# Performance work log

Hardware: AMD Instinct MI355X
Metric: run time of the kernel (lower is better)

Reference implementation:

```python
import math
import jax, jax.numpy as jnp
import numpy as np

T_MIN = 0.1
T_MAX = 1.0


def _log_cond_prob(energy, text_mask, mel_mask, direction, neg):
    # energy: (B, I, J); returns (B, I, J, K) with K=J (alpha) or J-1 (beta)
    B, I, J = energy.shape
    if direction == 'alpha':
        K = J
        tri_jk = jnp.arange(J)[:, None] >= jnp.arange(K)[None, :]  # torch triu: valid if j >= k
    else:
        K = J - 1
        tri_jk = jnp.arange(J)[:, None] <= jnp.arange(K)[None, :]  # torch tril: valid if j <= k
    tm = text_mask[:, :, None, None]           # (B,I,1,1)
    mmj = mel_mask[:, None, :, None]           # (B,1,J,1)
    mmk = mel_mask[:, None, None, :K]          # (B,1,1,K)
    mask = tm & mmj & mmk                      # (B,I,J,K)
    tri = tri_jk[None, None] & mask
    mask_invalid = jnp.broadcast_to(tm & mmk, (B, I, J, K))
    text_invalid = jnp.broadcast_to(tm, (B, I, J, K))
    right_mask = mask | (~mask_invalid)
    e = jnp.broadcast_to(energy[..., None], (B, I, J, K))
    e = jnp.where((~tri) & mask_invalid, neg, e)
    e = jnp.where(~mask_invalid, -10.0, e)
    e = e - jax.nn.logsumexp(e, axis=2, keepdims=True)  # normalize over mel dim j
    e = jnp.where(~mask_invalid, neg, e)
    e = jnp.where(~right_mask, -10.0, e)
    e = jnp.where(~text_invalid, -10.0, e)
    return e


def _roll(x, shifts, axis):
    # per-batch roll of x along `axis` by shifts[b]
    return jax.vmap(lambda xb, s: jnp.roll(xb, s, axis=axis - 1))(x, shifts)


def _right_shift(x, sh_t, sh_m):
    x = _roll(x, sh_t, 1)
    x = _roll(x, sh_m, 2)
    return _roll(x, sh_m.at[1:].add(-1), 3)  # faithful to in-place shifts_mel_dim[1:] -= 1


def _left_shift(x, sh_t, sh_m):
    x = x[..., None]
    x = _roll(x, -sh_t, 1)
    x = _roll(x, -sh_m, 2)
    return x[..., 0]


def _compute_alpha(lcp_a, neg):
    # alpha[:, i, j] = lse_k(alpha[:, i-1, k] + lcp_a[:, i-1, j-1, k]) for j >= i
    B, I, J, _ = lcp_a.shape
    j_idx = jnp.arange(J + 1)
    row0 = jnp.full((B, J + 1), neg, dtype=lcp_a.dtype).at[:, 0].set(0.0)

    def step(prev, xs):  # prev = alpha[:, i-1, :J]
        lcp_i, i = xs
        new = jax.nn.logsumexp(prev[:, None, :] + lcp_i, axis=2)  # (B, J), index j-1
        row = jnp.concatenate([jnp.full((B, 1), neg, dtype=new.dtype), new], axis=1)
        row = jnp.where(j_idx[None, :] >= i, row, neg)
        return row[:, :J], row

    _, rows = jax.lax.scan(step, row0[:, :J], (jnp.swapaxes(lcp_a, 0, 1), jnp.arange(1, I + 1)))
    return jnp.concatenate([row0[:, None, :], jnp.swapaxes(rows, 0, 1)], axis=1)  # (B, I+1, J+1)


def _compute_beta(lcp_b, neg):
    # beta[:, i, j] = lse_k(beta[:, i+1, k+1] + lcp_b[:, i, j, k]) for j < J+i-I+1
    B, I, J, _ = lcp_b.shape
    j_idx = jnp.arange(J)
    last = jnp.full((B, J), neg, dtype=lcp_b.dtype).at[:, J - 1].set(0.0)

    def step(nxt, xs):
        lcp_i, i = xs
        full = jax.nn.logsumexp(nxt[:, 1:][:, None, :] + lcp_i, axis=2)  # (B, J)
        row = jnp.where(j_idx[None, :] < (J + i - I + 1), full, neg)
        return row, row

    _, rows = jax.lax.scan(step, last, (jnp.swapaxes(lcp_b[:, :I - 1], 0, 1), jnp.arange(I - 1)), reverse=True)
    return jnp.concatenate([jnp.swapaxes(rows, 0, 1), last[:, None, :]], axis=1)  # (B, I, J)


def _forward(text_embeddings, mel_embeddings, text_mask, mel_mask, noise, temperature_ratio, neg):
    B, I, Dt = text_embeddings.shape
    _, J, Dm = mel_embeddings.shape
    energy = jnp.einsum('bid,bjd->bij', text_embeddings, mel_embeddings) / math.sqrt(Dt * Dm)
    temp = T_MIN + (T_MAX - T_MIN) * temperature_ratio[0]
    energy = (energy - jnp.log(-jnp.log(noise))) / temp  # Gumbel noise + temperature
    lcp_a = _log_cond_prob(energy, text_mask, mel_mask, 'alpha', neg)
    alpha = _compute_alpha(lcp_a, neg)
    t_len = text_mask.sum(1)
    m_len = mel_mask.sum(1)
    sh_t = t_len.max() - t_len
    sh_m = m_len.max() - m_len
    lcp_b = _log_cond_prob(energy, text_mask, mel_mask, 'beta', neg)
    lcp_b = _right_shift(lcp_b, sh_t, sh_m)
    beta = _compute_beta(lcp_b, neg)
    beta = _left_shift(beta, sh_t, sh_m)
    gamma = alpha[:, 1:, 1:] + beta
    gamma_mask = text_mask[:, :, None] & mel_mask[:, None, :]
    gls_mask = jnp.broadcast_to(text_mask[:, :, None], (B, I, J)) | gamma_mask
    gamma = jnp.where(gls_mask, gamma, neg)
    gamma = gamma - jax.nn.logsumexp(gamma, axis=1, keepdims=True)  # normalize over text dim
    gamma = jnp.where(gamma_mask, gamma, neg)
    expanded = jnp.einsum('bij,bid->bjd', jnp.exp(gamma), text_embeddings)
    expanded = expanded * mel_mask[:, :, None]
    return gamma, expanded


def setup_inputs() -> dict:
    key = jax.random.key(0)
    k1, k2, k3, k4 = jax.random.split(key, 4)
    B, I, J, Dt, Dm = 1, 128, 640, 256, 256
    text_embeddings = jax.random.normal(k1, (B, I, Dt), dtype=jnp.float32)
    mel_embeddings = jax.random.normal(k2, (B, J, Dm), dtype=jnp.float32)
    text_mask = jnp.ones((B, I), dtype=bool)
    mel_mask = jnp.ones((B, J), dtype=bool)
    noise = jnp.clip(jax.random.uniform(k3, (B, I, J), dtype=jnp.float32), 1e-8, 1.0 - 1e-8)
    temperature_ratio = jax.random.uniform(k4, (1,), dtype=jnp.float32)
    return {
        'text_embeddings': text_embeddings,
        'mel_embeddings': mel_embeddings,
        'text_mask': text_mask,
        'mel_mask': mel_mask,
        'noise': noise,
        'temperature_ratio': temperature_ratio,
    }


def reference(text_embeddings, mel_embeddings, text_mask, mel_mask, noise, temperature_ratio):
    return _forward(text_embeddings, mel_embeddings, text_mask, mel_mask, noise, temperature_ratio, -jnp.inf)
```

## Files before the change

kernel.cpp:

```cpp
#include <hip/hip_runtime.h>
#include <math.h>

constexpr int TI = 128;
constexpr int TJ = 640;
constexpr int TD = 256;
constexpr int EPL = 10;
constexpr int NS  = 3;
constexpr int CH  = 4;
constexpr int NP  = 6;

#define NEG (-1e30f)
#define LOG2E 1.44269504088896340736f
#define LN2   0.69314718055994530942f

__device__ __forceinline__ float rexp2(float x) { return __builtin_amdgcn_exp2f(x); }
__device__ __forceinline__ float rlog2(float x) { return __builtin_amdgcn_logf(x); }

struct MS { float m, s; };
__device__ __forceinline__ MS ms_combine(MS a, MS b) {
    float d = b.m - a.m;
    bool al = d <= 0.0f;
    float m = al ? a.m : b.m;
    float t = rexp2(al ? d : -d);
    float s = al ? fmaf(b.s, t, a.s) : fmaf(a.s, t, b.s);
    return {m, s};
}
__device__ __forceinline__ MS ms_push(MS run, float x) { return ms_combine(run, {x, 1.0f}); }
__device__ __forceinline__ float ms_final(MS a) {
    return (a.m < -1e29f) ? NEG : a.m + rlog2(a.s);
}

template<int CTRL, int RMASK>
__device__ __forceinline__ float dpp_f(float src, float oldv) {
    int r = __builtin_amdgcn_update_dpp(
        __float_as_int(oldv), __float_as_int(src), CTRL, RMASK, 0xF, false);
    return __int_as_float(r);
}
template<int CTRL, int RMASK>
__device__ __forceinline__ MS dpp_ms(MS v) {
    MS t;
    t.m = dpp_f<CTRL, RMASK>(v.m, NEG);
    t.s = dpp_f<CTRL, RMASK>(v.s, 0.0f);
    return t;
}
__device__ __forceinline__ MS wave_incl_scan_ms(MS v) {
    v = ms_combine(dpp_ms<0x111, 0xF>(v), v);
    v = ms_combine(dpp_ms<0x112, 0xF>(v), v);
    v = ms_combine(dpp_ms<0x114, 0xF>(v), v);
    v = ms_combine(dpp_ms<0x118, 0xF>(v), v);
    v = ms_combine(dpp_ms<0x142, 0xA>(v), v);
    v = ms_combine(dpp_ms<0x143, 0xC>(v), v);
    return v;
}
__device__ __forceinline__ MS wave_excl_from_incl_ms(MS incl) {
    return dpp_ms<0x138, 0xF>(incl);
}
__device__ __forceinline__ float wave_incl_scan_add(float v) {
    v += dpp_f<0x111, 0xF>(v, 0.0f);
    v += dpp_f<0x112, 0xF>(v, 0.0f);
    v += dpp_f<0x114, 0xF>(v, 0.0f);
    v += dpp_f<0x118, 0xF>(v, 0.0f);
    v += dpp_f<0x142, 0xA>(v, 0.0f);
    v += dpp_f<0x143, 0xC>(v, 0.0f);
    return v;
}
__device__ __forceinline__ float wave_incl_scan_max(float v) {
    v = fmaxf(v, dpp_f<0x111, 0xF>(v, NEG));
    v = fmaxf(v, dpp_f<0x112, 0xF>(v, NEG));
    v = fmaxf(v, dpp_f<0x114, 0xF>(v, NEG));
    v = fmaxf(v, dpp_f<0x118, 0xF>(v, NEG));
    v = fmaxf(v, dpp_f<0x142, 0xA>(v, NEG));
    v = fmaxf(v, dpp_f<0x143, 0xC>(v, NEG));
    return v;
}
__device__ __forceinline__ float readlane63(float v) {
    return __int_as_float(__builtin_amdgcn_readlane(__float_as_int(v), 63));
}
__device__ __forceinline__ float readlaneN(float v, int n) {
    return __int_as_float(__builtin_amdgcn_readlane(__float_as_int(v), n));
}

__device__ __forceinline__ void cbar() { asm volatile("" ::: "memory"); }
__device__ __forceinline__ int opaque_zero(int v) {
    int r;
    asm("v_xor_b32 %0, %1, %1" : "=v"(r) : "v"(v));
    return r;
}
__device__ __forceinline__ int pollwait(volatile int* flag, int need) {
    int rv;
    do { rv = *flag; } while (rv < need);
    return rv;
}

__device__ __forceinline__ void load10(float* d, const float* s) {
    const float2* p = (const float2*)s;
    #pragma unroll
    for (int k = 0; k < 5; k++) { float2 v = p[k]; d[2*k] = v.x; d[2*k+1] = v.y; }
}
__device__ __forceinline__ void store10(float* d, const float* v) {
    float2* p = (float2*)d;
    #pragma unroll
    for (int k = 0; k < 5; k++) { float2 t; t.x = v[2*k]; t.y = v[2*k+1]; p[k] = t; }
}

__global__ __launch_bounds__(256) void k_melT(
        const float* __restrict__ mel, float* __restrict__ melT) {
    __shared__ float ldsT[64][65];
    int j0 = blockIdx.x * 64, c0 = blockIdx.y * 64, tid = threadIdx.x;
    int rr = tid >> 4, c4 = tid & 15;
    #pragma unroll
    for (int p = 0; p < 4; p++) {
        int r = p * 16 + rr;
        float4 v = *(const float4*)(mel + (size_t)(j0 + r) * TD + c0 + c4 * 4);
        ldsT[c4 * 4 + 0][r] = v.x;
        ldsT[c4 * 4 + 1][r] = v.y;
        ldsT[c4 * 4 + 2][r] = v.z;
        ldsT[c4 * 4 + 3][r] = v.w;
    }
    __syncthreads();
    int jj = tid & 63, cw = tid >> 6;
    #pragma unroll
    for (int p = 0; p < 16; p++) {
        int cc = p * 4 + cw;
        melT[(size_t)(c0 + cc) * TJ + j0 + jj] = ldsT[cc][jj];
    }
}

__global__ __launch_bounds__(640) void k_energy(
        const float* __restrict__ text, const float* __restrict__ melT,
        const float* __restrict__ noise, const float* __restrict__ trat,
        float* __restrict__ energy, float* __restrict__ Ga,
        float* __restrict__ Gb, float* __restrict__ Cst) {
    __shared__ float trowm[TD], trowc[TD], trowp[TD];
    __shared__ float erowm[TJ], erowc[TJ], erowp[TJ];
    __shared__ float pcur[TJ], scur[TJ];
    __shared__ float wred[2][EPL];
    int i = blockIdx.x, tid = threadIdx.x;
    if (tid < TD) {
        trowc[tid] = text[i * TD + tid];
        trowm[tid] = (i > 0)      ? text[(i - 1) * TD + tid] : 0.0f;
        trowp[tid] = (i < TI - 1) ? text[(i + 1) * TD + tid] : 0.0f;
    }
    __syncthreads();
    float temp = 0.1f + 0.9f * trat[0];
    float sc = LOG2E / temp;
    int j = tid;
    float am = 0.0f, ac = 0.0f, ap = 0.0f;
    #pragma unroll 8
    for (int c = 0; c < TD; c++) {
        float m = melT[(size_t)c * TJ + j];
        am = fmaf(trowm[c], m, am);
        ac = fmaf(trowc[c], m, ac);
        ap = fmaf(trowp[c], m, ap);
    }
    float gm = (i > 0)      ? logf(-logf(noise[(i - 1) * TJ + j])) : 0.0f;
    float gc =                logf(-logf(noise[i * TJ + j]));
    float gp = (i < TI - 1) ? logf(-logf(noise[(i + 1) * TJ + j])) : 0.0f;
    erowm[j] = (am * (1.0f / 256.0f) - gm) * sc;
    float e2 = (ac * (1.0f / 256.0f) - gc) * sc;
    erowc[j] = e2;
    erowp[j] = (ap * (1.0f / 256.0f) - gp) * sc;
    energy[i * TJ + j] = e2;
    __syncthreads();
    if (tid < 64) {
        int l = tid;
        MS loc = {NEG, 0.0f};
        #pragma unroll
        for (int q = 0; q < EPL; q++) loc = ms_push(loc, erowc[l * EPL + q]);
        MS off = wave_excl_from_incl_ms(wave_incl_scan_ms(loc));
        MS run = off;
        #pragma unroll
        for (int q = 0; q < EPL; q++) {
            run = ms_push(run, erowc[l * EPL + q]);
            pcur[l * EPL + q] = ms_final(run);
        }
        loc = {NEG, 0.0f};
        #pragma unroll
        for (int q = 0; q < EPL; q++) loc = ms_push(loc, erowc[TJ - 1 - (l * EPL + q)]);
        off = wave_excl_from_incl_ms(wave_incl_scan_ms(loc));
        run = off;
        #pragma unroll
        for (int q = 0; q < EPL; q++) {
            int idx = TJ - 1 - (l * EPL + q);
            run = ms_push(run, erowc[idx]);
            scur[idx] = ms_final(run);
        }
    }
    __syncthreads();
    float ga, gb;
    if (i == 0) ga = (j == 0) ? -scur[0] : NEG;
    else        ga = (j == 0) ? NEG : erowm[j - 1] - scur[j];
    bool has_b = (i <= TI - 2);
    if (has_b) {
        if (i == TI - 2) gb = (j == 1) ? -pcur[TJ - 2] : NEG;
        else             gb = (j == 0) ? NEG : erowp[TJ - j] - pcur[TJ - 1 - j];
    } else gb = NEG;
    int wv = tid >> 6, l = tid & 63;
    float ma = readlane63(wave_incl_scan_max(ga));
    float mb = readlane63(wave_incl_scan_max(gb));
    if (l == 0) { wred[0][wv] = ma; wred[1][wv] = mb; }
    __syncthreads();
    float Ca = wred[0][0], Cb = wred[1][0];
    #pragma unroll
    for (int k = 1; k < EPL; k++) {
        Ca = fmaxf(Ca, wred[0][k]);
        Cb = fmaxf(Cb, wred[1][k]);
    }
    Ga[i * TJ + j] = rexp2(ga - Ca);
    if (has_b) Gb[i * TJ + j] = rexp2(gb - Cb);
    if (tid == 0) { Cst[i] = Ca; if (has_b) Cst[TI + i] = Cb; }
}

__global__ __launch_bounds__(320, 1) void k_scan(
        const float* __restrict__ energy, const float* __restrict__ Ga,
        const float* __restrict__ Gb, const float* __restrict__ Cst,
        float* __restrict__ a, float* __restrict__ b) {
    __shared__ float Gring[NS][CH][TJ];
    __shared__ float Ppring[NP][TJ + 8];
    __shared__ int ready[NS];
    __shared__ int prow, cdone, ocnt[2];
    const int tid = threadIdx.x, wave = tid >> 6, l = tid & 63;
    const bool is_alpha = (blockIdx.x == 0);
    const int nrows = is_alpha ? TI : TI - 1;
    const int nch = (nrows + CH - 1) / CH;
    if (tid < NS) ready[tid] = 0;
    if (tid == 0) { prow = 0; cdone = 0; ocnt[0] = 0; ocnt[1] = 0; }
    __syncthreads();

    if (wave == 0) {
        float C0, C1;
        if (is_alpha) { C0 = Cst[l]; C1 = Cst[64 + l]; }
        else          { C0 = Cst[128 + l]; C1 = Cst[192 + l]; }
        float Pp[EPL];
        #pragma unroll
        for (int q = 0; q < EPL; q++) Pp[q] = 0.0f;
        float rprev = 0.0f, Lam = 0.0f;
        int seen0 = 0, seen1 = 0;
        for (int c = 0; c < nch; c++) {
            int rv = pollwait(&ready[c % NS], c + 1);
            cbar();
            int tok = opaque_zero(rv);
            float Gr[CH][EPL];
            #pragma unroll
            for (int q = 0; q < CH; q++)
                if (c * CH + q < nrows)
                    load10(Gr[q], &Gring[c % NS][q][l * EPL + tok]);
            #pragma unroll
            for (int s = 0; s < CH; s++) {
                int t = c * CH + s;
                if (t < nrows) {
                    float lp[EPL];
                    if (t == 0) {
                        #pragma unroll
                        for (int q = 0; q < EPL; q++) lp[q] = Gr[0][q];
                    } else {
                        float carry = dpp_f<0x138, 0xF>(Pp[EPL - 1], 0.0f);
                        float rp = rprev;
                        lp[0] = carry * rp * Gr[s][0];
                        #pragma unroll
                        for (int q = 1; q < EPL; q++) lp[q] = Pp[q - 1] * rp * Gr[s][q];
                    }
                    #pragma unroll
                    for (int q = 9; q >= 1; q--) lp[q] += lp[q - 1];
                    #pragma unroll
                    for (int q = 9; q >= 2; q--) lp[q] += lp[q - 2];
                    #pragma unroll
                    for (int q = 9; q >= 4; q--) lp[q] += lp[q - 4];
                    #pragma unroll
                    for (int q = 9; q >= 8; q--) lp[q] += lp[q - 8];
                    float incl = wave_incl_scan_add(lp[EPL - 1]);
                    float excl = dpp_f<0x138, 0xF>(incl, 0.0f);
                    #pragma unroll
                    for (int q = 0; q < EPL; q++) Pp[q] = excl + lp[q];
                    float T = readlane63(incl);
                    int idx2 = is_alpha ? t : (126 - t);
                    float Cc = (idx2 < 64) ? readlaneN(C0, idx2) : readlaneN(C1, idx2 - 64);
                    float basev = Lam + Cc;
                    if (t >= NP) {
                        int need = ((t - NP) >> 1) + 1;
                        if (t & 1) {
                            if (seen1 < need) { seen1 = pollwait(&ocnt[1], need); cbar(); }
                        } else {
                            if (seen0 < need) { seen0 = pollwait(&ocnt[0], need); cbar(); }
                        }
                    }
                    int ps = t % NP;
                    store10(&Ppring[ps][l * EPL], Pp);
                    if (l == 0) Ppring[ps][TJ] = basev;
                    cbar();
                    if (l == 0) *(volatile int*)&prow = t + 1;
                    Lam = basev + rlog2(T);
                    rprev = (T > 0.0f) ? __builtin_amdgcn_rcpf(T) : 0.0f;
                }
            }
            cbar();
            if (l == 0) *(volatile int*)&cdone = c + 1;
        }
    } else if (wave <= 2) {
        const float* Gsrc = is_alpha ? Ga : Gb;
        for (int c = wave - 1; c < nch; c += 2) {
            if (c >= NS) { int dv = pollwait(&cdone, c - NS + 1); cbar(); (void)dv; }
            int slot = c % NS;
            int cnt = nrows - c * CH; if (cnt > CH) cnt = CH;
            int m0 = is_alpha ? c * CH : (TI - 2 - c * CH - (cnt - 1));
            const float4* src = (const float4*)(Gsrc + (size_t)m0 * TJ);
            int total4 = cnt * (TJ / 4);
            #pragma unroll
            for (int it = 0; it < CH * TJ / 4 / 64; it++) {
                int o4 = it * 64 + l;
                if (o4 < total4) {
                    float4 v = src[o4];
                    int ri = o4 / 160, c4 = o4 - ri * 160;
                    int s = is_alpha ? ri : (cnt - 1 - ri);
                    ((float4*)Gring[slot][s])[c4] = v;
                }
            }
            __threadfence_block();
            if (l == 0) *(volatile int*)&ready[slot] = c + 1;
        }
    } else {
        int w = wave - 3;
        if (!is_alpha && w == 0) {
            #pragma unroll
            for (int k = 0; k < EPL; k++) {
                int j = l + 64 * k;
                b[(TI - 1) * TJ + j] = (j == TJ - 1) ? 0.0f : NEG;
            }
        }
        for (int t = w; t < nrows; t += 2) {
            int row = is_alpha ? t : (TI - 2 - t);
            const float* Erow = energy + (size_t)row * TJ;
            float ev[EPL];
            #pragma unroll
            for (int k = 0; k < EPL; k++) ev[k] = Erow[l + 64 * k];
            int rv = pollwait(&prow, t + 1);
            cbar();
            int tok = opaque_zero(rv);
            int ps = t % NP;
            float base = Ppring[ps][TJ + tok];
            float ov[EPL];
            #pragma unroll
            for (int k = 0; k < EPL; k++) {
                int j = l + 64 * k;
                int pj = is_alpha ? j : (TJ - 1 - j);
                ov[k] = ev[k] + rlog2(Ppring[ps][pj + tok]) + base;
            }
            float* dst = (is_alpha ? a : b) + (size_t)row * TJ;
            #pragma unroll
            for (int k = 0; k < EPL; k++) dst[l + 64 * k] = ov[k];
            cbar();
            if (l == 0) *(volatile int*)&ocnt[w] = (t >> 1) + 1;
        }
    }
}

__global__ __launch_bounds__(256) void k_gamma(
        const float* __restrict__ a, const float* __restrict__ b,
        const float* __restrict__ text,
        float* __restrict__ outg, float* __restrict__ oute) {
    __shared__ float w128[TI];
    __shared__ float redm[2], reds[2];
    int j = blockIdx.x, tid = threadIdx.x;
    float gg = NEG;
    if (tid < TI) {
        float av = a[tid * TJ + j];
        float bv = b[tid * TJ + j];
        gg = (av < -1e29f || bv < -1e29f) ? NEG : av + bv;
        MS v = {gg, 1.0f};
        #pragma unroll
        for (int off = 32; off > 0; off >>= 1) {
            float om = __shfl_xor(v.m, off, 64);
            float os = __shfl_xor(v.s, off, 64);
            v = ms_combine(v, {om, os});
        }
        if ((tid & 63) == 0) { redm[tid >> 6] = v.m; reds[tid >> 6] = v.s; }
    }
    __syncthreads();
    float lse = ms_final(ms_combine({redm[0], reds[0]}, {redm[1], reds[1]}));
    if (tid < TI) {
        bool fin = gg > -1e29f;
        outg[tid * TJ + j] = fin ? (gg - lse) * LN2 : NEG;
        w128[tid] = fin ? rexp2(gg - lse) : 0.0f;
    }
    __syncthreads();
    float acc = 0.0f;
    #pragma unroll 8
    for (int ii = 0; ii < TI; ii++) acc += w128[ii] * text[ii * TD + tid];
    oute[(size_t)j * TD + tid] = acc;
}

extern "C" void kernel_launch(void* const* d_in, const int* in_sizes, int n_in,
                              void* d_out, int out_size, void* d_ws, size_t ws_size,
                              hipStream_t stream) {
    const float* text  = (const float*)d_in[0];
    const float* mel   = (const float*)d_in[1];
    const float* noise = (const float*)d_in[4];
    const float* trat  = (const float*)d_in[5];

    float* outg = (float*)d_out;
    float* oute = outg + TI * TJ;

    float* w      = (float*)d_ws;
    float* energy = w;
    float* Ga     = w + 1 * TI * TJ;
    float* Gb     = w + 2 * TI * TJ;
    float* Cst    = Gb + (size_t)(TI - 1) * TJ;
    float* melT   = w + 3 * TI * TJ;
    float* aArr   = w + 3 * TI * TJ;
    float* bArr   = w + 4 * TI * TJ;

    k_melT  <<<dim3(TJ / 64, TD / 64), 256, 0, stream>>>(mel, melT);
    k_energy<<<TI, TJ, 0, stream>>>(text, melT, noise, trat, energy, Ga, Gb, Cst);
    k_scan  <<<2, 320, 0, stream>>>(energy, Ga, Gb, Cst, aArr, bArr);
    k_gamma <<<TJ, 256, 0, stream>>>(aArr, bArr, text, outg, oute);
}
```

Before: 146.5 us.

## Move energy addition out of serial scan into gamma with transposed layouts

The scan kernel no longer loads energy rows and adds them. It writes only the log-sum part, transposed to j-major. The energy add and the boundary row of beta move into k_gamma, which now reads the transposed ET/LaT/LbT arrays contiguously per block instead of with stride TJ. This takes loads off the latency-critical two-block serial scan, but its stores become strided by TI (uncoalesced) and k_energy's energy store becomes strided too.

```diff
diff --git a/kernel.cpp b/kernel.cpp
--- a/kernel.cpp
+++ b/kernel.cpp
@@ -129,7 +129,7 @@
 __global__ __launch_bounds__(640) void k_energy(
         const float* __restrict__ text, const float* __restrict__ melT,
         const float* __restrict__ noise, const float* __restrict__ trat,
-        float* __restrict__ energy, float* __restrict__ Ga,
+        float* __restrict__ ET, float* __restrict__ Ga,
         float* __restrict__ Gb, float* __restrict__ Cst) {
     __shared__ float trowm[TD], trowc[TD], trowp[TD];
     __shared__ float erowm[TJ], erowc[TJ], erowp[TJ];
@@ -160,7 +160,7 @@
     float e2 = (ac * (1.0f / 256.0f) - gc) * sc;
     erowc[j] = e2;
     erowp[j] = (ap * (1.0f / 256.0f) - gp) * sc;
-    energy[i * TJ + j] = e2;
+    ET[(size_t)j * TI + i] = e2;
     __syncthreads();
     if (tid < 64) {
         int l = tid;
@@ -212,9 +212,9 @@
 }
 
 __global__ __launch_bounds__(320, 1) void k_scan(
-        const float* __restrict__ energy, const float* __restrict__ Ga,
-        const float* __restrict__ Gb, const float* __restrict__ Cst,
-        float* __restrict__ a, float* __restrict__ b) {
+        const float* __restrict__ Ga, const float* __restrict__ Gb,
+        const float* __restrict__ Cst,
+        float* __restrict__ LaT, float* __restrict__ LbT) {
     __shared__ float Gring[NS][CH][TJ];
     __shared__ float Ppring[NP][TJ + 8];
     __shared__ int ready[NS];
@@ -320,34 +320,20 @@
         }
     } else {
         int w = wave - 3;
-        if (!is_alpha && w == 0) {
-            #pragma unroll
-            for (int k = 0; k < EPL; k++) {
-                int j = l + 64 * k;
-                b[(TI - 1) * TJ + j] = (j == TJ - 1) ? 0.0f : NEG;
-            }
-        }
+        float* dst = is_alpha ? LaT : LbT;
         for (int t = w; t < nrows; t += 2) {
             int row = is_alpha ? t : (TI - 2 - t);
-            const float* Erow = energy + (size_t)row * TJ;
-            float ev[EPL];
-            #pragma unroll
-            for (int k = 0; k < EPL; k++) ev[k] = Erow[l + 64 * k];
             int rv = pollwait(&prow, t + 1);
             cbar();
             int tok = opaque_zero(rv);
             int ps = t % NP;
             float base = Ppring[ps][TJ + tok];
-            float ov[EPL];
             #pragma unroll
             for (int k = 0; k < EPL; k++) {
                 int j = l + 64 * k;
                 int pj = is_alpha ? j : (TJ - 1 - j);
-                ov[k] = ev[k] + rlog2(Ppring[ps][pj + tok]) + base;
+                dst[(size_t)j * TI + row] = rlog2(Ppring[ps][pj + tok]) + base;
             }
-            float* dst = (is_alpha ? a : b) + (size_t)row * TJ;
-            #pragma unroll
-            for (int k = 0; k < EPL; k++) dst[l + 64 * k] = ov[k];
             cbar();
             if (l == 0) *(volatile int*)&ocnt[w] = (t >> 1) + 1;
         }
@@ -355,16 +341,19 @@
 }
 
 __global__ __launch_bounds__(256) void k_gamma(
-        const float* __restrict__ a, const float* __restrict__ b,
-        const float* __restrict__ text,
+        const float* __restrict__ ET, const float* __restrict__ LaT,
+        const float* __restrict__ LbT, const float* __restrict__ text,
         float* __restrict__ outg, float* __restrict__ oute) {
     __shared__ float w128[TI];
     __shared__ float redm[2], reds[2];
     int j = blockIdx.x, tid = threadIdx.x;
     float gg = NEG;
     if (tid < TI) {
-        float av = a[tid * TJ + j];
-        float bv = b[tid * TJ + j];
+        float e2 = ET[(size_t)j * TI + tid];
+        float av = e2 + LaT[(size_t)j * TI + tid];
+        float bv;
+        if (tid == TI - 1) bv = (j == TJ - 1) ? 0.0f : NEG;
+        else               bv = e2 + LbT[(size_t)j * TI + tid];
         gg = (av < -1e29f || bv < -1e29f) ? NEG : av + bv;
         MS v = {gg, 1.0f};
         #pragma unroll
@@ -401,16 +390,16 @@
     float* oute = outg + TI * TJ;
 
     float* w      = (float*)d_ws;
-    float* energy = w;
+    float* ET     = w;
     float* Ga     = w + 1 * TI * TJ;
     float* Gb     = w + 2 * TI * TJ;
     float* Cst    = Gb + (size_t)(TI - 1) * TJ;
     float* melT   = w + 3 * TI * TJ;
-    float* aArr   = w + 3 * TI * TJ;
-    float* bArr   = w + 4 * TI * TJ;
+    float* LaT    = w + 3 * TI * TJ;
+    float* LbT    = w + 4 * TI * TJ;
 
     k_melT  <<<dim3(TJ / 64, TD / 64), 256, 0, stream>>>(mel, melT);
-    k_energy<<<TI, TJ, 0, stream>>>(text, melT, noise, trat, energy, Ga, Gb, Cst);
-    k_scan  <<<2, 320, 0, stream>>>(energy, Ga, Gb, Cst, aArr, bArr);
-    k_gamma <<<TJ, 256, 0, stream>>>(aArr, bArr, text, outg, oute);
-}
+    k_energy<<<TI, TJ, 0, stream>>>(text, melT, noise, trat, ET, Ga, Gb, Cst);
+    k_scan  <<<2, 320, 0, stream>>>(Ga, Gb, Cst, LaT, LbT);
+    k_gamma <<<TJ, 256, 0, stream>>>(ET, LaT, LbT, text, outg, oute);
+}
```

Measured after the change: 170.8 us. 16.6% more time.

## Merge four kernels into two using global-flag inter-block synchronization

Applied to the files above, without the earlier changes.

Folds the mel transpose into the energy kernel and the gamma pass into the scan kernel, with device-scope atomic flags and spin-waits replacing kernel boundaries. It also adds s_sleep back-off to the LDS poll loops. The aim is to remove two launch gaps and let noise log work overlap the transpose. The cost is a memset launch, and correctness depends on all blocks being co-resident so the spinning blocks cannot deadlock. Gamma blocks also sit idle while the serial scan runs.

```diff
diff --git a/kernel.cpp b/kernel.cpp
--- a/kernel.cpp
+++ b/kernel.cpp
@@ -8,6 +8,7 @@
 constexpr int NS  = 3;
 constexpr int CH  = 4;
 constexpr int NP  = 6;
+constexpr int GAMMA_BLKS = 254;
 
 #define NEG (-1e30f)
 #define LOG2E 1.44269504088896340736f
@@ -87,8 +88,8 @@
     return r;
 }
 __device__ __forceinline__ int pollwait(volatile int* flag, int need) {
-    int rv;
-    do { rv = *flag; } while (rv < need);
+    int rv = *flag;
+    while (rv < need) { __builtin_amdgcn_s_sleep(1); rv = *flag; }
     return rv;
 }
 
@@ -103,48 +104,63 @@
     for (int k = 0; k < 5; k++) { float2 t; t.x = v[2*k]; t.y = v[2*k+1]; p[k] = t; }
 }
 
-__global__ __launch_bounds__(256) void k_melT(
-        const float* __restrict__ mel, float* __restrict__ melT) {
-    __shared__ float ldsT[64][65];
-    int j0 = blockIdx.x * 64, c0 = blockIdx.y * 64, tid = threadIdx.x;
-    int rr = tid >> 4, c4 = tid & 15;
-    #pragma unroll
-    for (int p = 0; p < 4; p++) {
-        int r = p * 16 + rr;
-        float4 v = *(const float4*)(mel + (size_t)(j0 + r) * TD + c0 + c4 * 4);
-        ldsT[c4 * 4 + 0][r] = v.x;
-        ldsT[c4 * 4 + 1][r] = v.y;
-        ldsT[c4 * 4 + 2][r] = v.z;
-        ldsT[c4 * 4 + 3][r] = v.w;
-    }
-    __syncthreads();
-    int jj = tid & 63, cw = tid >> 6;
-    #pragma unroll
-    for (int p = 0; p < 16; p++) {
-        int cc = p * 4 + cw;
-        melT[(size_t)(c0 + cc) * TJ + j0 + jj] = ldsT[cc][jj];
-    }
-}
-
-__global__ __launch_bounds__(640) void k_energy(
-        const float* __restrict__ text, const float* __restrict__ melT,
+__global__ __launch_bounds__(640) void k_A(
+        const float* __restrict__ mel, const float* __restrict__ text,
         const float* __restrict__ noise, const float* __restrict__ trat,
-        float* __restrict__ energy, float* __restrict__ Ga,
-        float* __restrict__ Gb, float* __restrict__ Cst) {
+        float* __restrict__ melT, float* __restrict__ energy,
+        float* __restrict__ Ga, float* __restrict__ Gb,
+        float* __restrict__ Cst, int* __restrict__ flagA) {
+    int bid = blockIdx.x, tid = threadIdx.x;
+    if (bid < 40) {
+        __shared__ float ldsT[64][65];
+        int j0 = (bid % 10) * 64, c0 = (bid / 10) * 64;
+        #pragma unroll
+        for (int it = 0; it < 2; it++) {
+            int idx = it * 640 + tid;
+            if (idx < 1024) {
+                int r = idx >> 4, c4 = idx & 15;
+                float4 v = *(const float4*)(mel + (size_t)(j0 + r) * TD + c0 + c4 * 4);
+                ldsT[c4 * 4 + 0][r] = v.x;
+                ldsT[c4 * 4 + 1][r] = v.y;
+                ldsT[c4 * 4 + 2][r] = v.z;
+                ldsT[c4 * 4 + 3][r] = v.w;
+            }
+        }
+        __syncthreads();
+        #pragma unroll
+        for (int it = 0; it < 7; it++) {
+            int idx = it * 640 + tid;
+            if (idx < 4096) {
+                int cc = idx >> 6, jj = idx & 63;
+                melT[(size_t)(c0 + cc) * TJ + j0 + jj] = ldsT[cc][jj];
+            }
+        }
+        __threadfence();
+        __syncthreads();
+        if (tid == 0)
+            __hip_atomic_fetch_add(flagA, 1, __ATOMIC_RELEASE, __HIP_MEMORY_SCOPE_AGENT);
+        return;
+    }
     __shared__ float trowm[TD], trowc[TD], trowp[TD];
     __shared__ float erowm[TJ], erowc[TJ], erowp[TJ];
     __shared__ float pcur[TJ], scur[TJ];
     __shared__ float wred[2][EPL];
-    int i = blockIdx.x, tid = threadIdx.x;
+    int i = bid - 40, j = tid;
     if (tid < TD) {
         trowc[tid] = text[i * TD + tid];
         trowm[tid] = (i > 0)      ? text[(i - 1) * TD + tid] : 0.0f;
         trowp[tid] = (i < TI - 1) ? text[(i + 1) * TD + tid] : 0.0f;
     }
-    __syncthreads();
     float temp = 0.1f + 0.9f * trat[0];
     float sc = LOG2E / temp;
-    int j = tid;
+    float gm = (i > 0)      ? logf(-logf(noise[(i - 1) * TJ + j])) : 0.0f;
+    float gc =                logf(-logf(noise[i * TJ + j]));
+    float gp = (i < TI - 1) ? logf(-logf(noise[(i + 1) * TJ + j])) : 0.0f;
+    if (tid == 0) {
+        while (__hip_atomic_load(flagA, __ATOMIC_ACQUIRE, __HIP_MEMORY_SCOPE_AGENT) < 40)
+            __builtin_amdgcn_s_sleep(4);
+    }
+    __syncthreads();
     float am = 0.0f, ac = 0.0f, ap = 0.0f;
     #pragma unroll 8
     for (int c = 0; c < TD; c++) {
@@ -153,9 +169,6 @@
         ac = fmaf(trowc[c], m, ac);
         ap = fmaf(trowp[c], m, ap);
     }
-    float gm = (i > 0)      ? logf(-logf(noise[(i - 1) * TJ + j])) : 0.0f;
-    float gc =                logf(-logf(noise[i * TJ + j]));
-    float gp = (i < TI - 1) ? logf(-logf(noise[(i + 1) * TJ + j])) : 0.0f;
     erowm[j] = (am * (1.0f / 256.0f) - gm) * sc;
     float e2 = (ac * (1.0f / 256.0f) - gc) * sc;
     erowc[j] = e2;
@@ -211,182 +224,196 @@
     if (tid == 0) { Cst[i] = Ca; if (has_b) Cst[TI + i] = Cb; }
 }
 
-__global__ __launch_bounds__(320, 1) void k_scan(
+__global__ __launch_bounds__(320, 1) void k_B(
         const float* __restrict__ energy, const float* __restrict__ Ga,
         const float* __restrict__ Gb, const float* __restrict__ Cst,
-        float* __restrict__ a, float* __restrict__ b) {
-    __shared__ float Gring[NS][CH][TJ];
-    __shared__ float Ppring[NP][TJ + 8];
-    __shared__ int ready[NS];
-    __shared__ int prow, cdone, ocnt[2];
-    const int tid = threadIdx.x, wave = tid >> 6, l = tid & 63;
-    const bool is_alpha = (blockIdx.x == 0);
-    const int nrows = is_alpha ? TI : TI - 1;
-    const int nch = (nrows + CH - 1) / CH;
-    if (tid < NS) ready[tid] = 0;
-    if (tid == 0) { prow = 0; cdone = 0; ocnt[0] = 0; ocnt[1] = 0; }
-    __syncthreads();
-
-    if (wave == 0) {
-        float C0, C1;
-        if (is_alpha) { C0 = Cst[l]; C1 = Cst[64 + l]; }
-        else          { C0 = Cst[128 + l]; C1 = Cst[192 + l]; }
-        float Pp[EPL];
-        #pragma unroll
-        for (int q = 0; q < EPL; q++) Pp[q] = 0.0f;
-        float rprev = 0.0f, Lam = 0.0f;
-        int seen0 = 0, seen1 = 0;
-        for (int c = 0; c < nch; c++) {
-            int rv = pollwait(&ready[c % NS], c + 1);
-            cbar();
-            int tok = opaque_zero(rv);
-            float Gr[CH][EPL];
+        const float* __restrict__ text,
+        float* __restrict__ a, float* __restrict__ b,
+        float* __restrict__ outg, float* __restrict__ oute,
+        int* __restrict__ flagC) {
+    int bid = blockIdx.x, tid = threadIdx.x;
+    if (bid < 2) {
+        __shared__ float Gring[NS][CH][TJ];
+        __shared__ float Ppring[NP][TJ + 8];
+        __shared__ int ready[NS];
+        __shared__ int prow, cdone, ocnt[2];
+        const int wave = tid >> 6, l = tid & 63;
+        const bool is_alpha = (bid == 0);
+        const int nrows = is_alpha ? TI : TI - 1;
+        const int nch = (nrows + CH - 1) / CH;
+        if (tid < NS) ready[tid] = 0;
+        if (tid == 0) { prow = 0; cdone = 0; ocnt[0] = 0; ocnt[1] = 0; }
+        __syncthreads();
+
+        if (wave == 0) {
+            float C0, C1;
+            if (is_alpha) { C0 = Cst[l]; C1 = Cst[64 + l]; }
+            else          { C0 = Cst[128 + l]; C1 = Cst[192 + l]; }
+            float Pp[EPL];
             #pragma unroll
-            for (int q = 0; q < CH; q++)
-                if (c * CH + q < nrows)
-                    load10(Gr[q], &Gring[c % NS][q][l * EPL + tok]);
-            #pragma unroll
-            for (int s = 0; s < CH; s++) {
-                int t = c * CH + s;
-                if (t < nrows) {
-                    float lp[EPL];
-                    if (t == 0) {
+            for (int q = 0; q < EPL; q++) Pp[q] = 0.0f;
+            float rprev = 0.0f, Lam = 0.0f;
+            int seen0 = 0, seen1 = 0;
+            for (int c = 0; c < nch; c++) {
+                int rv = pollwait(&ready[c % NS], c + 1);
+                cbar();
+                int tok = opaque_zero(rv);
+                float Gr[CH][EPL];
+                #pragma unroll
+                for (int q = 0; q < CH; q++)
+                    if (c * CH + q < nrows)
+                        load10(Gr[q], &Gring[c % NS][q][l * EPL + tok]);
+                #pragma unroll
+                for (int s = 0; s < CH; s++) {
+                    int t = c * CH + s;
+                    if (t < nrows) {
+                        float lp[EPL];
+                        if (t == 0) {
+                            #pragma unroll
+                            for (int q = 0; q < EPL; q++) lp[q] = Gr[0][q];
+                        } else {
+                            float carry = dpp_f<0x138, 0xF>(Pp[EPL - 1], 0.0f);
+                            float rp = rprev;
+                            lp[0] = carry * rp * Gr[s][0];
+                            #pragma unroll
+                            for (int q = 1; q < EPL; q++) lp[q] = Pp[q - 1] * rp * Gr[s][q];
+                        }
                         #pragma unroll
-                        for (int q = 0; q < EPL; q++) lp[q] = Gr[0][q];
-                    } else {
-                        float carry = dpp_f<0x138, 0xF>(Pp[EPL - 1], 0.0f);
-                        float rp = rprev;
-                        lp[0] = carry * rp * Gr[s][0];
+                        for (int q = 9; q >= 1; q--) lp[q] += lp[q - 1];
                         #pragma unroll
-                        for (int q = 1; q < EPL; q++) lp[q] = Pp[q - 1] * rp * Gr[s][q];
+                        for (int q = 9; q >= 2; q--) lp[q] += lp[q - 2];
+                        #pragma unroll
+                        for (int q = 9; q >= 4; q--) lp[q] += lp[q - 4];
+                        #pragma unroll
+                        for (int q = 9; q >= 8; q--) lp[q] += lp[q - 8];
+                        float incl = wave_incl_scan_add(lp[EPL - 1]);
+                        float excl = dpp_f<0x138, 0xF>(incl, 0.0f);
+                        #pragma unroll
+                        for (int q = 0; q < EPL; q++) Pp[q] = excl + lp[q];
+                        float T = readlane63(incl);
+                        int idx2 = is_alpha ? t : (126 - t);
+                        float Cc = (idx2 < 64) ? readlaneN(C0, idx2) : readlaneN(C1, idx2 - 64);
+                        float basev = Lam + Cc;
+                        if (t >= NP) {
+                            int need = ((t - NP) >> 1) + 1;
+                            if (t & 1) {
+                                if (seen1 < need) { seen1 = pollwait(&ocnt[1], need); cbar(); }
+                            } else {
+                                if (seen0 < need) { seen0 = pollwait(&ocnt[0], need); cbar(); }
+                            }
+                        }
+                        int ps = t % NP;
+                        store10(&Ppring[ps][l * EPL], Pp);
+                        if (l == 0) Ppring[ps][TJ] = basev;
+                        cbar();
+                        if (l == 0) *(volatile int*)&prow = t + 1;
+                        Lam = basev + rlog2(T);
+                        rprev = (T > 0.0f) ? __builtin_amdgcn_rcpf(T) : 0.0f;
                     }
-                    #pragma unroll
-                    for (int q = 9; q >= 1; q--) lp[q] += lp[q - 1];
-                    #pragma unroll
-                    for (int q = 9; q >= 2; q--) lp[q] += lp[q - 2];
-                    #pragma unroll
-                    for (int q = 9; q >= 4; q--) lp[q] += lp[q - 4];
-                    #pragma unroll
-                    for (int q = 9; q >= 8; q--) lp[q] += lp[q - 8];
-                    float incl = wave_incl_scan_add(lp[EPL - 1]);
-                    float excl = dpp_f<0x138, 0xF>(incl, 0.0f);
-                    #pragma unroll
-                    for (int q = 0; q < EPL; q++) Pp[q] = excl + lp[q];
-                    float T = readlane63(incl);
-                    int idx2 = is_alpha ? t : (126 - t);
-                    float Cc = (idx2 < 64) ? readlaneN(C0, idx2) : readlaneN(C1, idx2 - 64);
-                    float basev = Lam + Cc;
-                    if (t >= NP) {
-                        int need = ((t - NP) >> 1) + 1;
-                        if (t & 1) {
-                            if (seen1 < need) { seen1 = pollwait(&ocnt[1], need); cbar(); }
-                        } else {
-                            if (seen0 < need) { seen0 = pollwait(&ocnt[0], need); cbar(); }
-                        }
+                }
+                cbar();
+                if (l == 0) *(volatile int*)&cdone = c + 1;
+            }
+        } else if (wave <= 2) {
+            const float* Gsrc = is_alpha ? Ga : Gb;
+            for (int c = wave - 1; c < nch; c += 2) {
+                if (c >= NS) { int dv = pollwait(&cdone, c - NS + 1); cbar(); (void)dv; }
+                int slot = c % NS;
+                int cnt = nrows - c * CH; if (cnt > CH) cnt = CH;
+                int m0 = is_alpha ? c * CH : (TI - 2 - c * CH - (cnt - 1));
+                const float4* src = (const float4*)(Gsrc + (size_t)m0 * TJ);
+                int total4 = cnt * (TJ / 4);
+                #pragma unroll
+                for (int it = 0; it < CH * TJ / 4 / 64; it++) {
+                    int o4 = it * 64 + l;
+                    if (o4 < total4) {
+                        float4 v = src[o4];
+                        int ri = o4 / 160, c4 = o4 - ri * 160;
+                        int s = is_alpha ? ri : (cnt - 1 - ri);
+                        ((float4*)Gring[slot][s])[c4] = v;
                     }
-                    int ps = t % NP;
-                    store10(&Ppring[ps][l * EPL], Pp);
-                    if (l == 0) Ppring[ps][TJ] = basev;
-                    cbar();
-                    if (l == 0) *(volatile int*)&prow = t + 1;
-                    Lam = basev + rlog2(T);
-                    rprev = (T > 0.0f) ? __builtin_amdgcn_rcpf(T) : 0.0f;
                 }
-            }
-            cbar();
-            if (l == 0) *(volatile int*)&cdone = c + 1;
-        }
-    } else if (wave <= 2) {
-        const float* Gsrc = is_alpha ? Ga : Gb;
-        for (int c = wave - 1; c < nch; c += 2) {
-            if (c >= NS) { int dv = pollwait(&cdone, c - NS + 1); cbar(); (void)dv; }
-            int slot = c % NS;
-            int cnt = nrows - c * CH; if (cnt > CH) cnt = CH;
-            int m0 = is_alpha ? c * CH : (TI - 2 - c * CH - (cnt - 1));
-            const float4* src = (const float4*)(Gsrc + (size_t)m0 * TJ);
-            int total4 = cnt * (TJ / 4);
-            #pragma unroll
-            for (int it = 0; it < CH * TJ / 4 / 64; it++) {
-                int o4 = it * 64 + l;
-                if (o4 < total4) {
-                    float4 v = src[o4];
-                    int ri = o4 / 160, c4 = o4 - ri * 160;
-                    int s = is_alpha ? ri : (cnt - 1 - ri);
-                    ((float4*)Gring[slot][s])[c4] = v;
+                __threadfence_block();
+                if (l == 0) *(volatile int*)&ready[slot] = c + 1;
+            }
+        } else {
+            int w = wave - 3;
+            if (!is_alpha && w == 0) {
+                #pragma unroll
+                for (int k = 0; k < EPL; k++) {
+                    int j = l + 64 * k;
+                    b[(TI - 1) * TJ + j] = (j == TJ - 1) ? 0.0f : NEG;
                 }
             }
-            __threadfence_block();
-            if (l == 0) *(volatile int*)&ready[slot] = c + 1;
-        }
-    } else {
-        int w = wave - 3;
-        if (!is_alpha && w == 0) {
-            #pragma unroll
-            for (int k = 0; k < EPL; k++) {
-                int j = l + 64 * k;
-                b[(TI - 1) * TJ + j] = (j == TJ - 1) ? 0.0f : NEG;
-            }
-        }
-        for (int t = w; t < nrows; t += 2) {
-            int row = is_alpha ? t : (TI - 2 - t);
-            const float* Erow = energy + (size_t)row * TJ;
-            float ev[EPL];
-            #pragma unroll
-            for (int k = 0; k < EPL; k++) ev[k] = Erow[l + 64 * k];
-            int rv = pollwait(&prow, t + 1);
-            cbar();
-            int tok = opaque_zero(rv);
-            int ps = t % NP;
-            float base = Ppring[ps][TJ + tok];
-            float ov[EPL];
-            #pragma unroll
-            for (int k = 0; k < EPL; k++) {
-                int j = l + 64 * k;
-                int pj = is_alpha ? j : (TJ - 1 - j);
-                ov[k] = ev[k] + rlog2(Ppring[ps][pj + tok]) + base;
-            }
-            float* dst = (is_alpha ? a : b) + (size_t)row * TJ;
-            #pragma unroll
-            for (int k = 0; k < EPL; k++) dst[l + 64 * k] = ov[k];
-            cbar();
-            if (l == 0) *(volatile int*)&ocnt[w] = (t >> 1) + 1;
-        }
-    }
-}
-
-__global__ __launch_bounds__(256) void k_gamma(
-        const float* __restrict__ a, const float* __restrict__ b,
-        const float* __restrict__ text,
-        float* __restrict__ outg, float* __restrict__ oute) {
+            for (int t = w; t < nrows; t += 2) {
+                int row = is_alpha ? t : (TI - 2 - t);
+                const float* Erow = energy + (size_t)row * TJ;
+                float ev[EPL];
+                #pragma unroll
+                for (int k = 0; k < EPL; k++) ev[k] = Erow[l + 64 * k];
+                int rv = pollwait(&prow, t + 1);
+                cbar();
+                int tok = opaque_zero(rv);
+                int ps = t % NP;
+                float base = Ppring[ps][TJ + tok];
+                float ov[EPL];
+                #pragma unroll
+                for (int k = 0; k < EPL; k++) {
+                    int j = l + 64 * k;
+                    int pj = is_alpha ? j : (TJ - 1 - j);
+                    ov[k] = ev[k] + rlog2(Ppring[ps][pj + tok]) + base;
+                }
+                float* dst = (is_alpha ? a : b) + (size_t)row * TJ;
+                #pragma unroll
+                for (int k = 0; k < EPL; k++) dst[l + 64 * k] = ov[k];
+                cbar();
+                if (l == 0) *(volatile int*)&ocnt[w] = (t >> 1) + 1;
+            }
+        }
+        __threadfence();
+        __syncthreads();
+        if (tid == 0)
+            __hip_atomic_fetch_add(flagC, 1, __ATOMIC_RELEASE, __HIP_MEMORY_SCOPE_AGENT);
+        return;
+    }
     __shared__ float w128[TI];
     __shared__ float redm[2], reds[2];
-    int j = blockIdx.x, tid = threadIdx.x;
-    float gg = NEG;
-    if (tid < TI) {
-        float av = a[tid * TJ + j];
-        float bv = b[tid * TJ + j];
-        gg = (av < -1e29f || bv < -1e29f) ? NEG : av + bv;
-        MS v = {gg, 1.0f};
-        #pragma unroll
-        for (int off = 32; off > 0; off >>= 1) {
-            float om = __shfl_xor(v.m, off, 64);
-            float os = __shfl_xor(v.s, off, 64);
-            v = ms_combine(v, {om, os});
-        }
-        if ((tid & 63) == 0) { redm[tid >> 6] = v.m; reds[tid >> 6] = v.s; }
+    if (tid == 0) {
+        while (__hip_atomic_load(flagC, __ATOMIC_ACQUIRE, __HIP_MEMORY_SCOPE_AGENT) < 2)
+            __builtin_amdgcn_s_sleep(4);
     }
     __syncthreads();
-    float lse = ms_final(ms_combine({redm[0], reds[0]}, {redm[1], reds[1]}));
-    if (tid < TI) {
-        bool fin = gg > -1e29f;
-        outg[tid * TJ + j] = fin ? (gg - lse) * LN2 : NEG;
-        w128[tid] = fin ? rexp2(gg - lse) : 0.0f;
-    }
-    __syncthreads();
-    float acc = 0.0f;
-    #pragma unroll 8
-    for (int ii = 0; ii < TI; ii++) acc += w128[ii] * text[ii * TD + tid];
-    oute[(size_t)j * TD + tid] = acc;
+    for (int j = bid - 2; j < TJ; j += GAMMA_BLKS) {
+        float gg = NEG;
+        if (tid < TI) {
+            float av = a[tid * TJ + j];
+            float bv = b[tid * TJ + j];
+            gg = (av < -1e29f || bv < -1e29f) ? NEG : av + bv;
+            MS v = {gg, 1.0f};
+            #pragma unroll
+            for (int off = 32; off > 0; off >>= 1) {
+                float om = __shfl_xor(v.m, off, 64);
+                float os = __shfl_xor(v.s, off, 64);
+                v = ms_combine(v, {om, os});
+            }
+            if ((tid & 63) == 0) { redm[tid >> 6] = v.m; reds[tid >> 6] = v.s; }
+        }
+        __syncthreads();
+        float lse = ms_final(ms_combine({redm[0], reds[0]}, {redm[1], reds[1]}));
+        if (tid < TI) {
+            bool fin = gg > -1e29f;
+            outg[tid * TJ + j] = fin ? (gg - lse) * LN2 : NEG;
+            w128[tid] = fin ? rexp2(gg - lse) : 0.0f;
+        }
+        __syncthreads();
+        if (tid < TD) {
+            float acc = 0.0f;
+            #pragma unroll 8
+            for (int ii = 0; ii < TI; ii++) acc += w128[ii] * text[ii * TD + tid];
+            oute[(size_t)j * TD + tid] = acc;
+        }
+        __syncthreads();
+    }
 }
 
 extern "C" void kernel_launch(void* const* d_in, const int* in_sizes, int n_in,
@@ -405,12 +432,14 @@
     float* Ga     = w + 1 * TI * TJ;
     float* Gb     = w + 2 * TI * TJ;
     float* Cst    = Gb + (size_t)(TI - 1) * TJ;
+    int*   flags  = (int*)(Cst + 320);
     float* melT   = w + 3 * TI * TJ;
     float* aArr   = w + 3 * TI * TJ;
     float* bArr   = w + 4 * TI * TJ;
 
-    k_melT  <<<dim3(TJ / 64, TD / 64), 256, 0, stream>>>(mel, melT);
-    k_energy<<<TI, TJ, 0, stream>>>(text, melT, noise, trat, energy, Ga, Gb, Cst);
-    k_scan  <<<2, 320, 0, stream>>>(energy, Ga, Gb, Cst, aArr, bArr);
-    k_gamma <<<TJ, 256, 0, stream>>>(aArr, bArr, text, outg, oute);
-}
+    hipMemsetAsync(flags, 0, 2 * sizeof(int), stream);
+    k_A<<<168, 640, 0, stream>>>(mel, text, noise, trat, melT, energy, Ga, Gb,
+                                 Cst, flags + 0);
+    k_B<<<2 + GAMMA_BLKS, 320, 0, stream>>>(energy, Ga, Gb, Cst, text,
+                                            aArr, bArr, outg, oute, flags + 1);
+}
```

New measurement: 441.9 us. 202% more time.

## Deepen scan ring buffer and process four mel columns per gamma block

Applied to the files above, without the earlier changes.

The scan kernel's producer/consumer ring grows from 6 to 12 slots, and the wait-parity logic is adjusted so the producer waits on the correct consumer wave. This lets the prefix-scan wave run further ahead of the output waves before stalling. The gamma kernel now handles four mel columns per block, using float4 loads and stores for a/b/gamma and reusing each text load across four accumulators. That cuts repeated text reads and the block count, at the cost of more LDS and registers per block and fewer blocks (160) to fill the GPU.

```diff
diff --git a/kernel.cpp b/kernel.cpp
--- a/kernel.cpp
+++ b/kernel.cpp
@@ -7,7 +7,7 @@
 constexpr int EPL = 10;
 constexpr int NS  = 3;
 constexpr int CH  = 4;
-constexpr int NP  = 6;
+constexpr int NP  = 12;
 
 #define NEG (-1e30f)
 #define LOG2E 1.44269504088896340736f
@@ -277,8 +277,9 @@
                     float Cc = (idx2 < 64) ? readlaneN(C0, idx2) : readlaneN(C1, idx2 - 64);
                     float basev = Lam + Cc;
                     if (t >= NP) {
-                        int need = ((t - NP) >> 1) + 1;
-                        if (t & 1) {
+                        int tf = t - NP;
+                        int need = (tf >> 1) + 1;
+                        if (tf & 1) {
                             if (seen1 < need) { seen1 = pollwait(&ocnt[1], need); cbar(); }
                         } else {
                             if (seen0 < need) { seen0 = pollwait(&ocnt[0], need); cbar(); }
@@ -358,35 +359,58 @@
         const float* __restrict__ a, const float* __restrict__ b,
         const float* __restrict__ text,
         float* __restrict__ outg, float* __restrict__ oute) {
-    __shared__ float w128[TI];
-    __shared__ float redm[2], reds[2];
-    int j = blockIdx.x, tid = threadIdx.x;
-    float gg = NEG;
+    __shared__ float w128[4][TI];
+    __shared__ float redm[4][2], reds[4][2];
+    int j0 = blockIdx.x * 4, tid = threadIdx.x;
+    float gg[4];
     if (tid < TI) {
-        float av = a[tid * TJ + j];
-        float bv = b[tid * TJ + j];
-        gg = (av < -1e29f || bv < -1e29f) ? NEG : av + bv;
-        MS v = {gg, 1.0f};
-        #pragma unroll
-        for (int off = 32; off > 0; off >>= 1) {
-            float om = __shfl_xor(v.m, off, 64);
-            float os = __shfl_xor(v.s, off, 64);
-            v = ms_combine(v, {om, os});
-        }
-        if ((tid & 63) == 0) { redm[tid >> 6] = v.m; reds[tid >> 6] = v.s; }
-    }
-    __syncthreads();
-    float lse = ms_final(ms_combine({redm[0], reds[0]}, {redm[1], reds[1]}));
+        float4 av4 = *(const float4*)(a + (size_t)tid * TJ + j0);
+        float4 bv4 = *(const float4*)(b + (size_t)tid * TJ + j0);
+        float avs[4] = {av4.x, av4.y, av4.z, av4.w};
+        float bvs[4] = {bv4.x, bv4.y, bv4.z, bv4.w};
+        #pragma unroll
+        for (int c = 0; c < 4; c++) {
+            float av = avs[c], bv = bvs[c];
+            gg[c] = (av < -1e29f || bv < -1e29f) ? NEG : av + bv;
+            MS v = {gg[c], 1.0f};
+            #pragma unroll
+            for (int off = 32; off > 0; off >>= 1) {
+                float om = __shfl_xor(v.m, off, 64);
+                float os = __shfl_xor(v.s, off, 64);
+                v = ms_combine(v, {om, os});
+            }
+            if ((tid & 63) == 0) { redm[c][tid >> 6] = v.m; reds[c][tid >> 6] = v.s; }
+        }
+    }
+    __syncthreads();
+    float lse[4];
+    #pragma unroll
+    for (int c = 0; c < 4; c++)
+        lse[c] = ms_final(ms_combine({redm[c][0], reds[c][0]}, {redm[c][1], reds[c][1]}));
     if (tid < TI) {
-        bool fin = gg > -1e29f;
-        outg[tid * TJ + j] = fin ? (gg - lse) * LN2 : NEG;
-        w128[tid] = fin ? rexp2(gg - lse) : 0.0f;
-    }
-    __syncthreads();
-    float acc = 0.0f;
-    #pragma unroll 8
-    for (int ii = 0; ii < TI; ii++) acc += w128[ii] * text[ii * TD + tid];
-    oute[(size_t)j * TD + tid] = acc;
+        float og[4];
+        #pragma unroll
+        for (int c = 0; c < 4; c++) {
+            bool fin = gg[c] > -1e29f;
+            og[c] = fin ? (gg[c] - lse[c]) * LN2 : NEG;
+            w128[c][tid] = fin ? rexp2(gg[c] - lse[c]) : 0.0f;
+        }
+        *(float4*)(outg + (size_t)tid * TJ + j0) = make_float4(og[0], og[1], og[2], og[3]);
+    }
+    __syncthreads();
+    float acc0 = 0.0f, acc1 = 0.0f, acc2 = 0.0f, acc3 = 0.0f;
+    #pragma unroll 4
+    for (int ii = 0; ii < TI; ii++) {
+        float tv = text[ii * TD + tid];
+        acc0 = fmaf(w128[0][ii], tv, acc0);
+        acc1 = fmaf(w128[1][ii], tv, acc1);
+        acc2 = fmaf(w128[2][ii], tv, acc2);
+        acc3 = fmaf(w128[3][ii], tv, acc3);
+    }
+    oute[(size_t)(j0 + 0) * TD + tid] = acc0;
+    oute[(size_t)(j0 + 1) * TD + tid] = acc1;
+    oute[(size_t)(j0 + 2) * TD + tid] = acc2;
+    oute[(size_t)(j0 + 3) * TD + tid] = acc3;
 }
 
 extern "C" void kernel_launch(void* const* d_in, const int* in_sizes, int n_in,
@@ -412,5 +436,5 @@
     k_melT  <<<dim3(TJ / 64, TD / 64), 256, 0, stream>>>(mel, melT);
     k_energy<<<TI, TJ, 0, stream>>>(text, melT, noise, trat, energy, Ga, Gb, Cst);
     k_scan  <<<2, 320, 0, stream>>>(energy, Ga, Gb, Cst, aArr, bArr);
-    k_gamma <<<TJ, 256, 0, stream>>>(aArr, bArr, text, outg, oute);
-}
+    k_gamma <<<TJ / 4, 256, 0, stream>>>(aArr, bArr, text, outg, oute);
+}
```

Measured after the change: 149.4 us. Within noise of the previous version (+2.0%).
